# Kernel tuning notes

Hardware: AMD Instinct MI355X
Metric: run time of the kernel (lower is better)

Reference implementation:

```python
import jax, jax.numpy as jnp
import numpy as np

# Mamba defaults (mamba_ssm): expand=2, d_state=16, d_conv=4, dt_rank=ceil(d_model/16)
D_MODEL = 256
DEPTH = 2
D_INNER = 2 * D_MODEL          # 512
D_STATE = 16
D_CONV = 4
DT_RANK = (D_MODEL + 15) // 16  # 16
BATCH = 2
SEQLEN = 2048


def setup_inputs() -> dict:
    key = jax.random.key(0)
    ks = jax.random.split(key, 12)
    s = 0.02
    x = jax.random.normal(ks[0], (BATCH, SEQLEN, D_MODEL), jnp.float32)
    ln_w = jnp.ones((DEPTH, D_MODEL), jnp.float32)
    ln_b = jnp.zeros((DEPTH, D_MODEL), jnp.float32)
    in_proj_w = jax.random.normal(ks[1], (DEPTH, 2 * D_INNER, D_MODEL), jnp.float32) * s
    conv_w = jax.random.normal(ks[2], (DEPTH, D_INNER, 1, D_CONV), jnp.float32) * 0.2
    conv_b = jnp.zeros((DEPTH, D_INNER), jnp.float32)
    x_proj_w = jax.random.normal(ks[3], (DEPTH, DT_RANK + 2 * D_STATE, D_INNER), jnp.float32) * s
    dt_proj_w = jax.random.normal(ks[4], (DEPTH, D_INNER, DT_RANK), jnp.float32) * (DT_RANK ** -0.5)
    # dt bias initialized so softplus(bias) ~ U(1e-3, 1e-1), as in mamba_ssm
    dt = jnp.exp(jax.random.uniform(ks[5], (DEPTH, D_INNER)) * (np.log(0.1) - np.log(1e-3)) + np.log(1e-3))
    dt_proj_b = dt + jnp.log(-jnp.expm1(-dt))  # inverse softplus
    A_log = jnp.log(jnp.broadcast_to(jnp.arange(1, D_STATE + 1, dtype=jnp.float32), (DEPTH, D_INNER, D_STATE)))
    D_param = jnp.ones((DEPTH, D_INNER), jnp.float32)
    out_proj_w = jax.random.normal(ks[6], (DEPTH, D_MODEL, D_INNER), jnp.float32) * s
    return {"x": x, "ln_w": ln_w, "ln_b": ln_b, "in_proj_w": in_proj_w,
            "conv_w": conv_w, "conv_b": conv_b, "x_proj_w": x_proj_w,
            "dt_proj_w": dt_proj_w, "dt_proj_b": dt_proj_b, "A_log": A_log,
            "D_param": D_param, "out_proj_w": out_proj_w}


def _layernorm(x, w, b, eps=1e-5):
    mu = jnp.mean(x, axis=-1, keepdims=True)
    var = jnp.var(x, axis=-1, keepdims=True)
    return (x - mu) * jax.lax.rsqrt(var + eps) * w + b


def _mamba_block(x, lw, lb, ipw, cw, cb, xpw, dpw, dpb, alog, dpar, opw):
    # x: [B, L, D]; returns x + Mamba(LN(x))  (residual handled by caller of stack)
    B, L, _ = x.shape
    h = _layernorm(x, lw, lb)
    xz = jnp.einsum('bld,ed->ble', h, ipw)            # [B, L, 2*d_inner]
    xi, z = jnp.split(xz, 2, axis=-1)
    # depthwise causal conv1d
    xc = jnp.transpose(xi, (0, 2, 1))                 # [B, d_inner, L]
    xc = jax.lax.conv_general_dilated(
        xc, cw, window_strides=(1,), padding=[(D_CONV - 1, 0)],
        feature_group_count=D_INNER, dimension_numbers=('NCH', 'OIH', 'NCH'))
    xc = jax.nn.silu(xc + cb[None, :, None])
    xc = jnp.transpose(xc, (0, 2, 1))                 # [B, L, d_inner]
    # input-dependent SSM parameters
    dbl = jnp.einsum('bld,ed->ble', xc, xpw)          # [B, L, dt_rank+2*d_state]
    dt = dbl[..., :DT_RANK]
    Bs = dbl[..., DT_RANK:DT_RANK + D_STATE]          # [B, L, d_state]
    Cs = dbl[..., DT_RANK + D_STATE:]                 # [B, L, d_state]
    delta = jax.nn.softplus(jnp.einsum('blr,dr->bld', dt, dpw) + dpb)  # [B, L, d_inner]
    A = -jnp.exp(alog)                                # [d_inner, d_state]
    dA = jnp.exp(jnp.einsum('bld,dn->bldn', delta, A))
    dBu = jnp.einsum('bld,bln,bld->bldn', delta, Bs, xc)
    # sequential selective scan over time (time-major)
    dA_t = jnp.moveaxis(dA, 1, 0)
    dBu_t = jnp.moveaxis(dBu, 1, 0)
    C_t = jnp.moveaxis(Cs, 1, 0)
    h0 = jnp.zeros((B, D_INNER, D_STATE), x.dtype)
    def step(hprev, inp):
        dA_, dBu_, C_ = inp
        hnew = dA_ * hprev + dBu_                     # [B, d_inner, d_state]
        y = jnp.einsum('bdn,bn->bd', hnew, C_)        # [B, d_inner]
        return hnew, y
    _, ys = jax.lax.scan(step, h0, (dA_t, dBu_t, C_t))
    y = jnp.moveaxis(ys, 0, 1)                        # [B, L, d_inner]
    y = y + xc * dpar
    y = y * jax.nn.silu(z)
    out = jnp.einsum('ble,de->bld', y, opw)           # [B, L, D]
    return x + out


def reference(x, ln_w, ln_b, in_proj_w, conv_w, conv_b, x_proj_w,
              dt_proj_w, dt_proj_b, A_log, D_param, out_proj_w):
    for i in range(DEPTH):
        x = _mamba_block(x, ln_w[i], ln_b[i], in_proj_w[i], conv_w[i], conv_b[i],
                         x_proj_w[i], dt_proj_w[i], dt_proj_b[i], A_log[i],
                         D_param[i], out_proj_w[i])
    return x
```

## Files before the change

kernel.cpp:

```cpp
#include <hip/hip_runtime.h>
#include <hip/hip_bf16.h>
#include <math.h>

#define D_MODEL 256
#define DEPTH 2
#define D_INNER 512
#define D_STATE 16
#define D_CONV 4
#define DT_RANK 16
#define BATCH 2
#define SEQLEN 2048
#define MROWS (BATCH * SEQLEN)

#define LCH 8
#define NCH 512
#define CPB 256

typedef __attribute__((ext_vector_type(8))) short bf16x8;
typedef __attribute__((ext_vector_type(4))) float f32x4;

__device__ __forceinline__ float silu(float v) {
    return v / (1.0f + __expf(-v));
}

__device__ __forceinline__ ushort f2bf(float f) {
    union { float f; unsigned u; } v; v.f = f;
    unsigned r = v.u + 0x7FFFu + ((v.u >> 16) & 1u);
    return (ushort)(r >> 16);
}

__device__ __forceinline__ float bf2f(ushort u) {
    union { unsigned u; float f; } v; v.u = ((unsigned)u) << 16;
    return v.f;
}

__device__ __forceinline__ float softplus_f(float x) {
    return (x > 20.f) ? x : __logf(1.f + __expf(x));
}

#define XS_STR 260
#define HS_STR 264
#define XC_STR 520

__global__ __launch_bounds__(256) void k_cvt(
    const float* __restrict__ ipw, const float* __restrict__ xpw,
    const float* __restrict__ opw, ushort* __restrict__ ipwB,
    ushort* __restrict__ xpwB, ushort* __restrict__ opwB)
{
    size_t tid = (size_t)blockIdx.x * 256 + threadIdx.x;
    {
        float4 v = ((const float4*)ipw)[tid];
        ushort4 o = { f2bf(v.x), f2bf(v.y), f2bf(v.z), f2bf(v.w) };
        ((ushort4*)ipwB)[tid] = o;
    }
    if (tid < 12288) {
        float4 v = ((const float4*)xpw)[tid];
        ushort4 o = { f2bf(v.x), f2bf(v.y), f2bf(v.z), f2bf(v.w) };
        ((ushort4*)xpwB)[tid] = o;
    }
    if (tid < 65536) {
        float4 v = ((const float4*)opw)[tid];
        ushort4 o = { f2bf(v.x), f2bf(v.y), f2bf(v.z), f2bf(v.w) };
        ((ushort4*)opwB)[tid] = o;
    }
}

__global__ __launch_bounds__(512, 4) void k_front(
    const float* __restrict__ xin, const float* __restrict__ lnwL,
    const float* __restrict__ lnbL, const ushort* __restrict__ ipwL,
    const float* __restrict__ cwL, const float* __restrict__ cbL,
    const ushort* __restrict__ xpwL, const float* __restrict__ dpwL,
    const float* __restrict__ dpbL, const float* __restrict__ alogL,
    ushort* __restrict__ zsB, ushort* __restrict__ xcB,
    float* __restrict__ dbl, float* __restrict__ Ssum,
    float* __restrict__ sdsum)
{
    const int t = threadIdx.x, bid = blockIdx.x;
    const int lane = t & 63, w = t >> 6, l15 = lane & 15, quad = lane >> 4;
    __shared__ float  xs[11 * XS_STR];
    __shared__ ushort hs[16 * HS_STR];
    __shared__ ushort xi_s[11 * 512];
    __shared__ ushort xc_s[16 * XC_STR];
    __shared__ float  dbl_s[8 * 52];
    int m0 = bid * LCH;

    for (int i = t; i < 11 * 64; i += 512) {
        int r = i >> 6, c = (i & 63) * 4;
        int grow = m0 - 3 + r; if (grow < 0) grow = 0;
        float4 v = *(const float4*)(xin + (size_t)grow * D_MODEL + c);
        *(float4*)&xs[r * XS_STR + c] = v;
    }
    __syncthreads();

    if (t < 11 * 16) {
        int r = t >> 4, ci = t & 15;
        float s = 0.f, sq = 0.f;
        #pragma unroll
        for (int k = 0; k < 16; k++) {
            float v = xs[r * XS_STR + ci + 16 * k];
            s += v; sq += v * v;
        }
        #pragma unroll
        for (int off = 1; off < 16; off <<= 1) {
            s  += __shfl_xor(s, off, 16);
            sq += __shfl_xor(sq, off, 16);
        }
        float mu  = s * (1.0f / 256.f);
        float var = sq * (1.0f / 256.f) - mu * mu;
        float rst = rsqrtf(var + 1e-5f);
        #pragma unroll
        for (int k = 0; k < 16; k++) {
            int c = ci + 16 * k;
            float v = (xs[r * XS_STR + c] - mu) * rst * lnwL[c] + lnbL[c];
            hs[r * HS_STR + c] = f2bf(v);
        }
    }
    __syncthreads();

    #pragma unroll
    for (int f = 0; f < 8; f++) {
        int n = w * 128 + f * 16 + l15;
        f32x4 acc = (f32x4){0.f, 0.f, 0.f, 0.f};
        for (int k0 = 0; k0 < D_MODEL; k0 += 32) {
            bf16x8 af = *(const bf16x8*)&hs[l15 * HS_STR + quad * 8 + k0];
            bf16x8 bw = *(const bf16x8*)(ipwL + (size_t)n * D_MODEL + quad * 8 + k0);
            acc = __builtin_amdgcn_mfma_f32_16x16x32_bf16(af, bw, acc, 0, 0, 0);
        }
        if (n < 512) {
            #pragma unroll
            for (int r2 = 0; r2 < 4; r2++) {
                int rl = quad * 4 + r2;
                if (rl < 11) xi_s[rl * 512 + n] = f2bf(acc[r2]);
            }
        } else {
            #pragma unroll
            for (int r2 = 0; r2 < 4; r2++) {
                int rl = quad * 4 + r2;
                if (rl >= 3 && rl < 11)
                    zsB[(size_t)(m0 + rl - 3) * D_INNER + (n - 512)] =
                        f2bf(silu(acc[r2]));
            }
        }
    }
    __syncthreads();

    {
        float4 cw4 = *(const float4*)(cwL + t * 4);
        float cbv = cbL[t];
        #pragma unroll
        for (int rl = 0; rl < LCH; rl++) {
            int l = (m0 + rl) & (SEQLEN - 1);
            float s = cbv;
            if (l >= 3) s = fmaf(cw4.x, bf2f(xi_s[(rl + 0) * 512 + t]), s);
            if (l >= 2) s = fmaf(cw4.y, bf2f(xi_s[(rl + 1) * 512 + t]), s);
            if (l >= 1) s = fmaf(cw4.z, bf2f(xi_s[(rl + 2) * 512 + t]), s);
            s = fmaf(cw4.w, bf2f(xi_s[(rl + 3) * 512 + t]), s);
            ushort xcv = f2bf(silu(s));
            xc_s[rl * XC_STR + t] = xcv;
            xcB[(size_t)(m0 + rl) * D_INNER + t] = xcv;
        }
    }
    __syncthreads();

    if (w < 3) {
        f32x4 acc = (f32x4){0.f, 0.f, 0.f, 0.f};
        for (int k0 = 0; k0 < D_INNER; k0 += 32) {
            bf16x8 af = *(const bf16x8*)&xc_s[l15 * XC_STR + quad * 8 + k0];
            bf16x8 bw = *(const bf16x8*)(xpwL + (size_t)(w * 16 + l15) * D_INNER + quad * 8 + k0);
            acc = __builtin_amdgcn_mfma_f32_16x16x32_bf16(af, bw, acc, 0, 0, 0);
        }
        int n = w * 16 + l15;
        #pragma unroll
        for (int r2 = 0; r2 < 4; r2++) {
            int rl = quad * 4 + r2;
            if (rl < LCH) {
                dbl_s[rl * 52 + n] = acc[r2];
                dbl[(size_t)(m0 + rl) * 48 + n] = acc[r2];
            }
        }
    }
    __syncthreads();

    {
        float a[16], wdp[16];
        #pragma unroll
        for (int n = 0; n < 16; n++) a[n] = -__expf(alogL[(size_t)t * 16 + n]);
        *(float4*)&wdp[0]  = *(const float4*)(dpwL + (size_t)t * 16 + 0);
        *(float4*)&wdp[4]  = *(const float4*)(dpwL + (size_t)t * 16 + 4);
        *(float4*)&wdp[8]  = *(const float4*)(dpwL + (size_t)t * 16 + 8);
        *(float4*)&wdp[12] = *(const float4*)(dpwL + (size_t)t * 16 + 12);
        float bias = dpbL[t];
        float h[16];
        #pragma unroll
        for (int n = 0; n < 16; n++) h[n] = 0.f;
        float sd = 0.f;
        for (int j = 0; j < LCH; j++) {
            const float* dp = &dbl_s[j * 52];
            float dot = bias;
            #pragma unroll
            for (int r2 = 0; r2 < 16; r2++) dot = fmaf(dp[r2], wdp[r2], dot);
            float dl = softplus_f(dot);
            float xv = bf2f(xc_s[j * XC_STR + t]);
            float u = dl * xv;
            sd += dl;
            #pragma unroll
            for (int n = 0; n < 16; n++)
                h[n] = fmaf(__expf(dl * a[n]), h[n], dp[16 + n] * u);
        }
        size_t sbase = (size_t)bid * 16 * D_INNER + t;
        #pragma unroll
        for (int n = 0; n < 16; n++) Ssum[sbase + (size_t)n * D_INNER] = h[n];
        sdsum[(size_t)bid * D_INNER + t] = sd;
    }
}

__global__ __launch_bounds__(512, 4) void k_comb(
    const float* __restrict__ alogL, const float* __restrict__ sdsum,
    float* __restrict__ Ssum)
{
    const int t = threadIdx.x, bid = blockIdx.x;
    __shared__ float S_l[32][17], sd_l[32][17];
    int ch32 = t & 31, seg = t >> 5;
    int chain = bid * 32 + ch32;
    int d = chain & 511;
    int n = (chain >> 9) & 15;
    int b = chain >> 13;
    float a = -__expf(alogL[(size_t)d * 16 + n]);
    int c0 = b * CPB + seg * 16;

    float s_r[16], sd_r[16];
    float S = 0.f, sdt = 0.f;
    #pragma unroll
    for (int j = 0; j < 16; j++) {
        size_t c = (size_t)(c0 + j);
        float s  = Ssum[(c * 16 + n) * D_INNER + d];
        float sd = sdsum[c * D_INNER + d];
        s_r[j] = s; sd_r[j] = sd;
        S = fmaf(__expf(a * sd), S, s);
        sdt += sd;
    }
    S_l[ch32][seg] = S;
    sd_l[ch32][seg] = sdt;
    __syncthreads();

    if (t < 32) {
        float hi = 0.f;
        #pragma unroll
        for (int g = 0; g < 16; g++) {
            float Sv = S_l[t][g], sdv = sd_l[t][g];
            S_l[t][g] = hi;
            hi = fmaf(__expf(a * sdv), hi, Sv);
        }
    }
    __syncthreads();

    float hi = S_l[ch32][seg];
    #pragma unroll
    for (int j = 0; j < 16; j++) {
        size_t c = (size_t)(c0 + j);
        Ssum[(c * 16 + n) * D_INNER + d] = hi;
        hi = fmaf(__expf(a * sd_r[j]), hi, s_r[j]);
    }
}

__global__ __launch_bounds__(512) void k_back(
    const float* __restrict__ dbl, const ushort* __restrict__ xcB,
    const ushort* __restrict__ zsB, const float* __restrict__ Ssum,
    const float* __restrict__ dpwL, const float* __restrict__ dpbL,
    const float* __restrict__ alogL, const float* __restrict__ dparL,
    const ushort* __restrict__ opwL, const float* __restrict__ xin,
    float* __restrict__ xout)
{
    const int t = threadIdx.x, bid = blockIdx.x;
    const int lane = t & 63, w = t >> 6, l15 = lane & 15, quad = lane >> 4;
    __shared__ ushort yy_s[16 * XC_STR];
    int m0 = bid * LCH;

    {
        float a[16], wdp[16];
        #pragma unroll
        for (int n = 0; n < 16; n++) a[n] = -__expf(alogL[(size_t)t * 16 + n]);
        *(float4*)&wdp[0]  = *(const float4*)(dpwL + (size_t)t * 16 + 0);
        *(float4*)&wdp[4]  = *(const float4*)(dpwL + (size_t)t * 16 + 4);
        *(float4*)&wdp[8]  = *(const float4*)(dpwL + (size_t)t * 16 + 8);
        *(float4*)&wdp[12] = *(const float4*)(dpwL + (size_t)t * 16 + 12);
        float bias = dpbL[t];
        float Dd = dparL[t];
        float h[16];
        size_t sbase = (size_t)bid * 16 * D_INNER + t;
        #pragma unroll
        for (int n = 0; n < 16; n++) h[n] = Ssum[sbase + (size_t)n * D_INNER];
        for (int j = 0; j < LCH; j++) {
            int row = m0 + j;
            const float* dp = dbl + (size_t)row * 48;
            float dot = bias;
            #pragma unroll
            for (int q = 0; q < 4; q++) {
                float4 dv = *(const float4*)(dp + q * 4);
                dot = fmaf(dv.x, wdp[4 * q + 0], dot);
                dot = fmaf(dv.y, wdp[4 * q + 1], dot);
                dot = fmaf(dv.z, wdp[4 * q + 2], dot);
                dot = fmaf(dv.w, wdp[4 * q + 3], dot);
            }
            float dl = softplus_f(dot);
            float xv = bf2f(xcB[(size_t)row * D_INNER + t]);
            float gate = bf2f(zsB[(size_t)row * D_INNER + t]);
            float u = dl * xv;
            float y0 = 0.f, y1 = 0.f, y2 = 0.f, y3 = 0.f;
            #pragma unroll
            for (int q = 0; q < 4; q++) {
                float4 Bv = *(const float4*)(dp + 16 + q * 4);
                float4 Cv = *(const float4*)(dp + 32 + q * 4);
                h[4 * q + 0] = fmaf(__expf(dl * a[4 * q + 0]), h[4 * q + 0], Bv.x * u);
                h[4 * q + 1] = fmaf(__expf(dl * a[4 * q + 1]), h[4 * q + 1], Bv.y * u);
                h[4 * q + 2] = fmaf(__expf(dl * a[4 * q + 2]), h[4 * q + 2], Bv.z * u);
                h[4 * q + 3] = fmaf(__expf(dl * a[4 * q + 3]), h[4 * q + 3], Bv.w * u);
                y0 = fmaf(h[4 * q + 0], Cv.x, y0);
                y1 = fmaf(h[4 * q + 1], Cv.y, y1);
                y2 = fmaf(h[4 * q + 2], Cv.z, y2);
                y3 = fmaf(h[4 * q + 3], Cv.w, y3);
            }
            float y = (y0 + y1) + (y2 + y3) + xv * Dd;
            yy_s[j * XC_STR + t] = f2bf(y * gate);
        }
    }
    __syncthreads();

    #pragma unroll
    for (int f = 0; f < 2; f++) {
        int n = w * 32 + f * 16 + l15;
        f32x4 acc = (f32x4){0.f, 0.f, 0.f, 0.f};
        for (int k0 = 0; k0 < D_INNER; k0 += 32) {
            bf16x8 af = *(const bf16x8*)&yy_s[l15 * XC_STR + quad * 8 + k0];
            bf16x8 bw = *(const bf16x8*)(opwL + (size_t)n * D_INNER + quad * 8 + k0);
            acc = __builtin_amdgcn_mfma_f32_16x16x32_bf16(af, bw, acc, 0, 0, 0);
        }
        #pragma unroll
        for (int r2 = 0; r2 < 4; r2++) {
            int rl = quad * 4 + r2;
            if (rl < LCH) {
                int row = m0 + rl;
                xout[(size_t)row * D_MODEL + n] =
                    acc[r2] + xin[(size_t)row * D_MODEL + n];
            }
        }
    }
}

extern "C" void kernel_launch(void* const* d_in, const int* in_sizes, int n_in,
                              void* d_out, int out_size, void* d_ws, size_t ws_size,
                              hipStream_t stream)
{
    const float* x    = (const float*)d_in[0];
    const float* lnw  = (const float*)d_in[1];
    const float* lnb  = (const float*)d_in[2];
    const float* ipw  = (const float*)d_in[3];
    const float* cw   = (const float*)d_in[4];
    const float* cb   = (const float*)d_in[5];
    const float* xpw  = (const float*)d_in[6];
    const float* dpw  = (const float*)d_in[7];
    const float* dpb  = (const float*)d_in[8];
    const float* alog = (const float*)d_in[9];
    const float* dpar = (const float*)d_in[10];
    const float* opw  = (const float*)d_in[11];
    float* out = (float*)d_out;

    char* p = (char*)d_ws;
    auto alloc = [&](size_t bytes) { char* r = p; p += (bytes + 255) & ~(size_t)255; return r; };
    ushort* zsB   = (ushort*)alloc((size_t)MROWS * D_INNER * 2);
    ushort* xcB   = (ushort*)alloc((size_t)MROWS * D_INNER * 2);
    float*  dbl   = (float*)alloc((size_t)MROWS * 48 * 4);
    float*  Ssum  = (float*)alloc((size_t)NCH * 16 * D_INNER * 4);
    float*  sdsum = (float*)alloc((size_t)NCH * D_INNER * 4);
    ushort* ipwB  = (ushort*)alloc((size_t)DEPTH * 2 * D_INNER * D_MODEL * 2);
    ushort* xpwB  = (ushort*)alloc((size_t)DEPTH * 48 * D_INNER * 2);
    ushort* opwB  = (ushort*)alloc((size_t)DEPTH * D_MODEL * D_INNER * 2);

    k_cvt<<<512, 256, 0, stream>>>(ipw, xpw, opw, ipwB, xpwB, opwB);

    for (int lyr = 0; lyr < DEPTH; lyr++) {
        const float* xin = (lyr == 0) ? x : out;
        float* xout = out;
        const float* alogL = alog + (size_t)lyr * D_INNER * D_STATE;
        const float* dpwL  = dpw + (size_t)lyr * D_INNER * DT_RANK;
        const float* dpbL  = dpb + lyr * D_INNER;

        k_front<<<NCH, 512, 0, stream>>>(
            xin, lnw + lyr * D_MODEL, lnb + lyr * D_MODEL,
            ipwB + (size_t)lyr * 2 * D_INNER * D_MODEL,
            cw + (size_t)lyr * D_INNER * D_CONV, cb + lyr * D_INNER,
            xpwB + (size_t)lyr * 48 * D_INNER, dpwL, dpbL, alogL,
            zsB, xcB, dbl, Ssum, sdsum);

        k_comb<<<512, 512, 0, stream>>>(alogL, sdsum, Ssum);

        k_back<<<NCH, 512, 0, stream>>>(
            dbl, xcB, zsB, Ssum, dpwL, dpbL, alogL,
            dpar + lyr * D_INNER,
            opwB + (size_t)lyr * D_MODEL * D_INNER, xin, xout);
    }
}
```

Baseline: 239.9 us.

## Pre-tile bf16 weights into MFMA fragment layout and batch fragment loads

The weight conversion kernel now writes in_proj, x_proj and out_proj weights in a 16x32 tile-contiguous layout, so each wave's MFMA B-fragment loads hit contiguous 1KB blocks. The GEMMs in k_front and k_back are restructured to preload A fragments (or B fragments) into registers and interleave several independent accumulators, which raises instruction-level parallelism. k_back also stages the per-chunk dbl rows in shared memory, the dt dot products use two partial sums, and launch bounds drop to 3 waves-per-EU occupancy to make room for the extra registers. The cost is higher register pressure and lower occupancy.

```diff
diff --git a/kernel.cpp b/kernel.cpp
--- a/kernel.cpp
+++ b/kernel.cpp
@@ -44,32 +44,41 @@
 
 __global__ __launch_bounds__(256) void k_cvt(
     const float* __restrict__ ipw, const float* __restrict__ xpw,
-    const float* __restrict__ opw, ushort* __restrict__ ipwB,
-    ushort* __restrict__ xpwB, ushort* __restrict__ opwB)
+    const float* __restrict__ opw, ushort* __restrict__ ipwT,
+    ushort* __restrict__ xpwT, ushort* __restrict__ opwT)
 {
     size_t tid = (size_t)blockIdx.x * 256 + threadIdx.x;
     {
-        float4 v = ((const float4*)ipw)[tid];
+        int lyr = (int)(tid >> 16), rem = (int)(tid & 65535);
+        int n = rem >> 6, k = (rem & 63) * 4;
+        float4 v = *(const float4*)(ipw + ((size_t)lyr * 1024 + n) * 256 + k);
+        int nt = n >> 4, r = n & 15, kt = k >> 5, c = k & 31;
         ushort4 o = { f2bf(v.x), f2bf(v.y), f2bf(v.z), f2bf(v.w) };
-        ((ushort4*)ipwB)[tid] = o;
+        *(ushort4*)(ipwT + (size_t)lyr * 262144 + (nt * 8 + kt) * 512 + r * 32 + c) = o;
     }
     if (tid < 12288) {
-        float4 v = ((const float4*)xpw)[tid];
+        int lyr = (int)(tid / 6144), rem = (int)(tid % 6144);
+        int n = rem >> 7, k = (rem & 127) * 4;
+        float4 v = *(const float4*)(xpw + ((size_t)lyr * 48 + n) * 512 + k);
+        int nt = n >> 4, r = n & 15, kt = k >> 5, c = k & 31;
         ushort4 o = { f2bf(v.x), f2bf(v.y), f2bf(v.z), f2bf(v.w) };
-        ((ushort4*)xpwB)[tid] = o;
+        *(ushort4*)(xpwT + (size_t)lyr * 24576 + (nt * 16 + kt) * 512 + r * 32 + c) = o;
     }
     if (tid < 65536) {
-        float4 v = ((const float4*)opw)[tid];
+        int lyr = (int)(tid >> 15), rem = (int)(tid & 32767);
+        int n = rem >> 7, k = (rem & 127) * 4;
+        float4 v = *(const float4*)(opw + ((size_t)lyr * 256 + n) * 512 + k);
+        int nt = n >> 4, r = n & 15, kt = k >> 5, c = k & 31;
         ushort4 o = { f2bf(v.x), f2bf(v.y), f2bf(v.z), f2bf(v.w) };
-        ((ushort4*)opwB)[tid] = o;
-    }
-}
-
-__global__ __launch_bounds__(512, 4) void k_front(
+        *(ushort4*)(opwT + (size_t)lyr * 131072 + (nt * 16 + kt) * 512 + r * 32 + c) = o;
+    }
+}
+
+__global__ __launch_bounds__(512, 3) void k_front(
     const float* __restrict__ xin, const float* __restrict__ lnwL,
-    const float* __restrict__ lnbL, const ushort* __restrict__ ipwL,
+    const float* __restrict__ lnbL, const ushort* __restrict__ ipwT,
     const float* __restrict__ cwL, const float* __restrict__ cbL,
-    const ushort* __restrict__ xpwL, const float* __restrict__ dpwL,
+    const ushort* __restrict__ xpwT, const float* __restrict__ dpwL,
     const float* __restrict__ dpbL, const float* __restrict__ alogL,
     ushort* __restrict__ zsB, ushort* __restrict__ xcB,
     float* __restrict__ dbl, float* __restrict__ Ssum,
@@ -117,28 +126,40 @@
     }
     __syncthreads();
 
-    #pragma unroll
-    for (int f = 0; f < 8; f++) {
-        int n = w * 128 + f * 16 + l15;
-        f32x4 acc = (f32x4){0.f, 0.f, 0.f, 0.f};
-        for (int k0 = 0; k0 < D_MODEL; k0 += 32) {
-            bf16x8 af = *(const bf16x8*)&hs[l15 * HS_STR + quad * 8 + k0];
-            bf16x8 bw = *(const bf16x8*)(ipwL + (size_t)n * D_MODEL + quad * 8 + k0);
-            acc = __builtin_amdgcn_mfma_f32_16x16x32_bf16(af, bw, acc, 0, 0, 0);
-        }
-        if (n < 512) {
-            #pragma unroll
-            for (int r2 = 0; r2 < 4; r2++) {
-                int rl = quad * 4 + r2;
-                if (rl < 11) xi_s[rl * 512 + n] = f2bf(acc[r2]);
-            }
-        } else {
-            #pragma unroll
-            for (int r2 = 0; r2 < 4; r2++) {
-                int rl = quad * 4 + r2;
-                if (rl >= 3 && rl < 11)
-                    zsB[(size_t)(m0 + rl - 3) * D_INNER + (n - 512)] =
-                        f2bf(silu(acc[r2]));
+    {
+        bf16x8 af[8];
+        #pragma unroll
+        for (int k8 = 0; k8 < 8; k8++)
+            af[k8] = *(const bf16x8*)&hs[l15 * HS_STR + quad * 8 + k8 * 32];
+        f32x4 acc[8];
+        #pragma unroll
+        for (int f = 0; f < 8; f++) acc[f] = (f32x4){0.f, 0.f, 0.f, 0.f};
+        const ushort* wb = ipwT + (size_t)w * 64 * 512 + l15 * 32 + quad * 8;
+        #pragma unroll
+        for (int k8 = 0; k8 < 8; k8++) {
+            #pragma unroll
+            for (int f = 0; f < 8; f++) {
+                bf16x8 bw = *(const bf16x8*)(wb + (f * 8 + k8) * 512);
+                acc[f] = __builtin_amdgcn_mfma_f32_16x16x32_bf16(af[k8], bw, acc[f], 0, 0, 0);
+            }
+        }
+        #pragma unroll
+        for (int f = 0; f < 8; f++) {
+            int n = w * 128 + f * 16 + l15;
+            if (n < 512) {
+                #pragma unroll
+                for (int r2 = 0; r2 < 4; r2++) {
+                    int rl = quad * 4 + r2;
+                    if (rl < 11) xi_s[rl * 512 + n] = f2bf(acc[f][r2]);
+                }
+            } else {
+                #pragma unroll
+                for (int r2 = 0; r2 < 4; r2++) {
+                    int rl = quad * 4 + r2;
+                    if (rl >= 3 && rl < 11)
+                        zsB[(size_t)(m0 + rl - 3) * D_INNER + (n - 512)] =
+                            f2bf(silu(acc[f][r2]));
+                }
             }
         }
     }
@@ -163,11 +184,16 @@
     __syncthreads();
 
     if (w < 3) {
+        const ushort* wb = xpwT + (size_t)w * 16 * 512 + l15 * 32 + quad * 8;
+        bf16x8 bw[16];
+        #pragma unroll
+        for (int k8 = 0; k8 < 16; k8++)
+            bw[k8] = *(const bf16x8*)(wb + k8 * 512);
         f32x4 acc = (f32x4){0.f, 0.f, 0.f, 0.f};
-        for (int k0 = 0; k0 < D_INNER; k0 += 32) {
-            bf16x8 af = *(const bf16x8*)&xc_s[l15 * XC_STR + quad * 8 + k0];
-            bf16x8 bw = *(const bf16x8*)(xpwL + (size_t)(w * 16 + l15) * D_INNER + quad * 8 + k0);
-            acc = __builtin_amdgcn_mfma_f32_16x16x32_bf16(af, bw, acc, 0, 0, 0);
+        #pragma unroll
+        for (int k8 = 0; k8 < 16; k8++) {
+            bf16x8 af = *(const bf16x8*)&xc_s[l15 * XC_STR + quad * 8 + k8 * 32];
+            acc = __builtin_amdgcn_mfma_f32_16x16x32_bf16(af, bw[k8], acc, 0, 0, 0);
         }
         int n = w * 16 + l15;
         #pragma unroll
@@ -196,10 +222,13 @@
         float sd = 0.f;
         for (int j = 0; j < LCH; j++) {
             const float* dp = &dbl_s[j * 52];
-            float dot = bias;
-            #pragma unroll
-            for (int r2 = 0; r2 < 16; r2++) dot = fmaf(dp[r2], wdp[r2], dot);
-            float dl = softplus_f(dot);
+            float d0 = 0.f, d1 = 0.f;
+            #pragma unroll
+            for (int r2 = 0; r2 < 8; r2++) {
+                d0 = fmaf(dp[r2], wdp[r2], d0);
+                d1 = fmaf(dp[8 + r2], wdp[8 + r2], d1);
+            }
+            float dl = softplus_f(bias + d0 + d1);
             float xv = bf2f(xc_s[j * XC_STR + t]);
             float u = dl * xv;
             sd += dl;
@@ -263,18 +292,22 @@
     }
 }
 
-__global__ __launch_bounds__(512) void k_back(
+__global__ __launch_bounds__(512, 3) void k_back(
     const float* __restrict__ dbl, const ushort* __restrict__ xcB,
     const ushort* __restrict__ zsB, const float* __restrict__ Ssum,
     const float* __restrict__ dpwL, const float* __restrict__ dpbL,
     const float* __restrict__ alogL, const float* __restrict__ dparL,
-    const ushort* __restrict__ opwL, const float* __restrict__ xin,
+    const ushort* __restrict__ opwT, const float* __restrict__ xin,
     float* __restrict__ xout)
 {
     const int t = threadIdx.x, bid = blockIdx.x;
     const int lane = t & 63, w = t >> 6, l15 = lane & 15, quad = lane >> 4;
     __shared__ ushort yy_s[16 * XC_STR];
+    __shared__ float  dbl_l[8 * 48];
     int m0 = bid * LCH;
+
+    if (t < 8 * 48) dbl_l[t] = dbl[(size_t)m0 * 48 + t];
+    __syncthreads();
 
     {
         float a[16], wdp[16];
@@ -292,33 +325,28 @@
         for (int n = 0; n < 16; n++) h[n] = Ssum[sbase + (size_t)n * D_INNER];
         for (int j = 0; j < LCH; j++) {
             int row = m0 + j;
-            const float* dp = dbl + (size_t)row * 48;
-            float dot = bias;
-            #pragma unroll
-            for (int q = 0; q < 4; q++) {
-                float4 dv = *(const float4*)(dp + q * 4);
-                dot = fmaf(dv.x, wdp[4 * q + 0], dot);
-                dot = fmaf(dv.y, wdp[4 * q + 1], dot);
-                dot = fmaf(dv.z, wdp[4 * q + 2], dot);
-                dot = fmaf(dv.w, wdp[4 * q + 3], dot);
-            }
-            float dl = softplus_f(dot);
+            const float* dp = &dbl_l[j * 48];
+            float d0 = 0.f, d1 = 0.f;
+            #pragma unroll
+            for (int r2 = 0; r2 < 8; r2++) {
+                d0 = fmaf(dp[r2], wdp[r2], d0);
+                d1 = fmaf(dp[8 + r2], wdp[8 + r2], d1);
+            }
+            float dl = softplus_f(bias + d0 + d1);
             float xv = bf2f(xcB[(size_t)row * D_INNER + t]);
             float gate = bf2f(zsB[(size_t)row * D_INNER + t]);
             float u = dl * xv;
             float y0 = 0.f, y1 = 0.f, y2 = 0.f, y3 = 0.f;
             #pragma unroll
             for (int q = 0; q < 4; q++) {
-                float4 Bv = *(const float4*)(dp + 16 + q * 4);
-                float4 Cv = *(const float4*)(dp + 32 + q * 4);
-                h[4 * q + 0] = fmaf(__expf(dl * a[4 * q + 0]), h[4 * q + 0], Bv.x * u);
-                h[4 * q + 1] = fmaf(__expf(dl * a[4 * q + 1]), h[4 * q + 1], Bv.y * u);
-                h[4 * q + 2] = fmaf(__expf(dl * a[4 * q + 2]), h[4 * q + 2], Bv.z * u);
-                h[4 * q + 3] = fmaf(__expf(dl * a[4 * q + 3]), h[4 * q + 3], Bv.w * u);
-                y0 = fmaf(h[4 * q + 0], Cv.x, y0);
-                y1 = fmaf(h[4 * q + 1], Cv.y, y1);
-                y2 = fmaf(h[4 * q + 2], Cv.z, y2);
-                y3 = fmaf(h[4 * q + 3], Cv.w, y3);
+                h[4 * q + 0] = fmaf(__expf(dl * a[4 * q + 0]), h[4 * q + 0], dp[16 + 4 * q + 0] * u);
+                h[4 * q + 1] = fmaf(__expf(dl * a[4 * q + 1]), h[4 * q + 1], dp[16 + 4 * q + 1] * u);
+                h[4 * q + 2] = fmaf(__expf(dl * a[4 * q + 2]), h[4 * q + 2], dp[16 + 4 * q + 2] * u);
+                h[4 * q + 3] = fmaf(__expf(dl * a[4 * q + 3]), h[4 * q + 3], dp[16 + 4 * q + 3] * u);
+                y0 = fmaf(h[4 * q + 0], dp[32 + 4 * q + 0], y0);
+                y1 = fmaf(h[4 * q + 1], dp[32 + 4 * q + 1], y1);
+                y2 = fmaf(h[4 * q + 2], dp[32 + 4 * q + 2], y2);
+                y3 = fmaf(h[4 * q + 3], dp[32 + 4 * q + 3], y3);
             }
             float y = (y0 + y1) + (y2 + y3) + xv * Dd;
             yy_s[j * XC_STR + t] = f2bf(y * gate);
@@ -326,22 +354,33 @@
     }
     __syncthreads();
 
-    #pragma unroll
-    for (int f = 0; f < 2; f++) {
-        int n = w * 32 + f * 16 + l15;
-        f32x4 acc = (f32x4){0.f, 0.f, 0.f, 0.f};
-        for (int k0 = 0; k0 < D_INNER; k0 += 32) {
-            bf16x8 af = *(const bf16x8*)&yy_s[l15 * XC_STR + quad * 8 + k0];
-            bf16x8 bw = *(const bf16x8*)(opwL + (size_t)n * D_INNER + quad * 8 + k0);
-            acc = __builtin_amdgcn_mfma_f32_16x16x32_bf16(af, bw, acc, 0, 0, 0);
-        }
-        #pragma unroll
-        for (int r2 = 0; r2 < 4; r2++) {
-            int rl = quad * 4 + r2;
-            if (rl < LCH) {
-                int row = m0 + rl;
-                xout[(size_t)row * D_MODEL + n] =
-                    acc[r2] + xin[(size_t)row * D_MODEL + n];
+    {
+        bf16x8 af[16];
+        #pragma unroll
+        for (int k8 = 0; k8 < 16; k8++)
+            af[k8] = *(const bf16x8*)&yy_s[l15 * XC_STR + quad * 8 + k8 * 32];
+        f32x4 acc0 = (f32x4){0.f, 0.f, 0.f, 0.f};
+        f32x4 acc1 = (f32x4){0.f, 0.f, 0.f, 0.f};
+        const ushort* wb = opwT + (size_t)w * 2 * 16 * 512 + l15 * 32 + quad * 8;
+        #pragma unroll
+        for (int k8 = 0; k8 < 16; k8++) {
+            bf16x8 b0 = *(const bf16x8*)(wb + k8 * 512);
+            bf16x8 b1 = *(const bf16x8*)(wb + (16 + k8) * 512);
+            acc0 = __builtin_amdgcn_mfma_f32_16x16x32_bf16(af[k8], b0, acc0, 0, 0, 0);
+            acc1 = __builtin_amdgcn_mfma_f32_16x16x32_bf16(af[k8], b1, acc1, 0, 0, 0);
+        }
+        #pragma unroll
+        for (int f = 0; f < 2; f++) {
+            int n = w * 32 + f * 16 + l15;
+            const f32x4& acc = (f == 0) ? acc0 : acc1;
+            #pragma unroll
+            for (int r2 = 0; r2 < 4; r2++) {
+                int rl = quad * 4 + r2;
+                if (rl < LCH) {
+                    int row = m0 + rl;
+                    xout[(size_t)row * D_MODEL + n] =
+                        acc[r2] + xin[(size_t)row * D_MODEL + n];
+                }
             }
         }
     }
@@ -372,11 +411,11 @@
     float*  dbl   = (float*)alloc((size_t)MROWS * 48 * 4);
     float*  Ssum  = (float*)alloc((size_t)NCH * 16 * D_INNER * 4);
     float*  sdsum = (float*)alloc((size_t)NCH * D_INNER * 4);
-    ushort* ipwB  = (ushort*)alloc((size_t)DEPTH * 2 * D_INNER * D_MODEL * 2);
-    ushort* xpwB  = (ushort*)alloc((size_t)DEPTH * 48 * D_INNER * 2);
-    ushort* opwB  = (ushort*)alloc((size_t)DEPTH * D_MODEL * D_INNER * 2);
-
-    k_cvt<<<512, 256, 0, stream>>>(ipw, xpw, opw, ipwB, xpwB, opwB);
+    ushort* ipwT  = (ushort*)alloc((size_t)DEPTH * 262144 * 2);
+    ushort* xpwT  = (ushort*)alloc((size_t)DEPTH * 24576 * 2);
+    ushort* opwT  = (ushort*)alloc((size_t)DEPTH * 131072 * 2);
+
+    k_cvt<<<512, 256, 0, stream>>>(ipw, xpw, opw, ipwT, xpwT, opwT);
 
     for (int lyr = 0; lyr < DEPTH; lyr++) {
         const float* xin = (lyr == 0) ? x : out;
@@ -387,9 +426,9 @@
 
         k_front<<<NCH, 512, 0, stream>>>(
             xin, lnw + lyr * D_MODEL, lnb + lyr * D_MODEL,
-            ipwB + (size_t)lyr * 2 * D_INNER * D_MODEL,
+            ipwT + (size_t)lyr * 262144,
             cw + (size_t)lyr * D_INNER * D_CONV, cb + lyr * D_INNER,
-            xpwB + (size_t)lyr * 48 * D_INNER, dpwL, dpbL, alogL,
+            xpwT + (size_t)lyr * 24576, dpwL, dpbL, alogL,
             zsB, xcB, dbl, Ssum, sdsum);
 
         k_comb<<<512, 512, 0, stream>>>(alogL, sdsum, Ssum);
@@ -397,6 +436,6 @@
         k_back<<<NCH, 512, 0, stream>>>(
             dbl, xcB, zsB, Ssum, dpwL, dpbL, alogL,
             dpar + lyr * D_INNER,
-            opwB + (size_t)lyr * D_MODEL * D_INNER, xin, xout);
-    }
-}
+            opwT + (size_t)lyr * 131072, xin, xout);
+    }
+}
```

New measurement: 207.6 us. 1.16x faster.
